# Kernel optimization log

Measured on AMD Instinct MI355X. Metric: run time of the kernel, lower is better.

Reference implementation:

```python
import jax, jax.numpy as jnp
import numpy as np

L, V, D = 8, 512, 256            # num_loci, per-locus vocab, embedding_dim
B, K = 8192, 16                  # batch, candidates per sample
HID = 2 * D                      # pooling MLP hidden width


def setup_inputs() -> dict:
    key = jax.random.key(0)
    k_tok, k_tab, k_w1, k_w2 = jax.random.split(key, 4)
    haplotypes = jax.random.randint(k_tok, (B, K, L), 0, V, dtype=jnp.int64)
    # nn.Embedding default init: N(0, 1); padding_idx row zeroed.
    tables = jax.random.normal(k_tab, (L, V, D), dtype=jnp.float32)
    tables = tables.at[:, 0, :].set(0.0)
    # Xavier-uniform for the two Linear layers (stored as [in, out]).
    lim1 = float(np.sqrt(6.0 / (L * D + HID)))
    W1 = jax.random.uniform(k_w1, (L * D, HID), jnp.float32, -lim1, lim1)
    b1 = jnp.zeros((HID,), jnp.float32)
    lim2 = float(np.sqrt(6.0 / (HID + D)))
    W2 = jax.random.uniform(k_w2, (HID, D), jnp.float32, -lim2, lim2)
    b2 = jnp.zeros((D,), jnp.float32)
    return {"haplotypes": haplotypes, "tables": tables,
            "W1": W1, "b1": b1, "W2": W2, "b2": b2}


def reference(haplotypes, tables, W1, b1, W2, b2):
    b, k, num_loci = haplotypes.shape
    vocab = tables.shape[1]
    tok = jnp.clip(haplotypes.reshape(-1, num_loci), 0, vocab - 1)  # [N, L]
    # Per-locus gather, vectorized over loci: [N, L, D]
    emb = tables[jnp.arange(num_loci), tok]
    # padding_idx row is all-zeros; masking keeps forward identical and
    # matches torch's zero-gradient behavior for the padding row.
    emb = emb * (tok != 0)[..., None].astype(emb.dtype)
    x = emb.reshape(emb.shape[0], num_loci * tables.shape[2])  # concat -> [N, L*D]
    h = jax.nn.gelu(x @ W1 + b1, approximate=False)            # torch GELU = erf
    out = h @ W2 + b2                                          # [N, D]
    return out.reshape(b, k, tables.shape[2])
```

## Files before the change

kernel.cpp:

```cpp
#include <hip/hip_runtime.h>
#include <math.h>

typedef __attribute__((ext_vector_type(8))) short  short8;
typedef __attribute__((ext_vector_type(4))) float  floatx4;
typedef __attribute__((ext_vector_type(2))) float  float2v;
typedef __attribute__((ext_vector_type(4))) unsigned int uintx4;

#define NLOCI 8
#define VOCAB 512
#define DDIM  256
#define HID   512
#define NSAMP (8192 * 16)

__device__ __forceinline__ float bitsf(unsigned int u) {
    union { unsigned int u; float f; } c; c.u = u; return c.f;
}
__device__ __forceinline__ unsigned short f2bf(float f) {
    union { float f; unsigned int u; } c; c.f = f;
    unsigned int u = c.u;
    return (unsigned short)((u + 0x7FFFu + ((u >> 16) & 1u)) >> 16);
}
__device__ __forceinline__ unsigned short f2bf_fast(float f) {
    union { float f; unsigned int u; } c; c.f = f;
    return (unsigned short)((c.u + 0x8000u) >> 16);
}
__device__ __forceinline__ float gelu_fast(float x) {
    float t = x * x;
    float y = x * __builtin_fmaf(0.035677408f, t, 0.79788456f);
    float e = __builtin_amdgcn_exp2f(y * 2.8853901f);
    float r = __builtin_amdgcn_rcpf(e + 1.0f);
    return x - x * r;
}
__device__ __forceinline__ void async_copy16(const void* g, void* l) {
    __builtin_amdgcn_global_load_lds(
        (const __attribute__((address_space(1))) unsigned int*)g,
        (__attribute__((address_space(3))) unsigned int*)l, 16, 0, 0);
}

__global__ __launch_bounds__(256) void k_prep(
    const float* __restrict__ tables,
    const float* __restrict__ W1,
    const float* __restrict__ b1,
    const float* __restrict__ W2,
    unsigned short* __restrict__ Tp,
    unsigned short* __restrict__ W2t)
{
    __shared__ unsigned short a_lds[64 * 256];
    __shared__ unsigned short bt_lds[64 * 256];

    const int t = threadIdx.x;

    if (blockIdx.x >= 512) {
        const int bid = blockIdx.x - 512;
        const int r0 = (bid & 7) * 64;
        const int c0 = (bid >> 3) * 64;
        float* tile = (float*)a_lds;
#pragma unroll
        for (int i = 0; i < 16; ++i) {
            int flat = i * 256 + t;
            int rr = flat >> 6, cc = flat & 63;
            tile[rr * 65 + cc] = W2[(r0 + rr) * DDIM + c0 + cc];
        }
        __syncthreads();
#pragma unroll
        for (int i = 0; i < 8; ++i) {
            int flat = i * 256 + t;
            int cc = flat >> 5, rp = (flat & 31) * 2;
            ushort2 v;
            v.x = f2bf(tile[rp * 65 + cc]);
            v.y = f2bf(tile[(rp + 1) * 65 + cc]);
            *(ushort2*)(W2t + (c0 + cc) * HID + r0 + rp) = v;
        }
        return;
    }

    const int l  = blockIdx.x >> 6;
    const int v0 = ((blockIdx.x >> 3) & 7) * 64;
    const int n0 = (blockIdx.x & 7) * 64;

    {
        const float* asrc = tables + (l * 512 + v0) * 256;
#pragma unroll
        for (int i = 0; i < 16; ++i) {
            int flat = i * 1024 + t * 4;
            int row = flat >> 8, k = flat & 255;
            float4 v = *(const float4*)(asrc + flat);
            ushort4 pk4;
            pk4.x = f2bf(v.x); pk4.y = f2bf(v.y); pk4.z = f2bf(v.z); pk4.w = f2bf(v.w);
            int chunkX = (k >> 3) ^ (row & 31);
            *(ushort4*)(a_lds + row * 256 + chunkX * 8 + (k & 7)) = pk4;
        }
    }
    {
        const int n = t & 63;
        const int kq = (t >> 6) * 64;
        const float* bsrc = W1 + (l * 256) * 512 + n0 + n;
#pragma unroll
        for (int i = 0; i < 8; ++i) {
            int k0 = kq + i * 8;
            short8 pk8;
#pragma unroll
            for (int j = 0; j < 8; ++j)
                pk8[j] = (short)f2bf(bsrc[(k0 + j) * 512]);
            int chunkX = (k0 >> 3) ^ (n & 31);
            *(short8*)(bt_lds + n * 256 + chunkX * 8) = pk8;
        }
    }
    __syncthreads();

    const int wave = t >> 6, lane = t & 63;
    const int p = lane & 15, q = lane >> 4;
    const int arow = wave * 16 + p;

    floatx4 acc[4];
#pragma unroll
    for (int nt = 0; nt < 4; ++nt) acc[nt] = (floatx4){0.f, 0.f, 0.f, 0.f};

#pragma unroll
    for (int kc = 0; kc < 8; ++kc) {
        int cq = kc * 4 + q;
        short8 afrag = *(const short8*)(a_lds + arow * 256 + (cq ^ (arow & 31)) * 8);
#pragma unroll
        for (int nt = 0; nt < 4; ++nt) {
            int brow = nt * 16 + p;
            short8 bfrag = *(const short8*)(bt_lds + brow * 256 + (cq ^ (brow & 31)) * 8);
            acc[nt] = __builtin_amdgcn_mfma_f32_16x16x32_bf16(afrag, bfrag, acc[nt], 0, 0, 0);
        }
    }

#pragma unroll
    for (int nt = 0; nt < 4; ++nt) {
        int col = n0 + nt * 16 + p;
        float badd = (l == 0) ? b1[col] : 0.0f;
#pragma unroll
        for (int r = 0; r < 4; ++r) {
            int row = v0 + wave * 16 + q * 4 + r;
            Tp[(l * 512 + row) * 512 + col] = f2bf(acc[nt][r] + badd);
        }
    }
}

__global__ __launch_bounds__(256, 3) void k_main(
    const int* __restrict__ hap,
    const unsigned short* __restrict__ Tp,
    const unsigned short* __restrict__ W2t,
    const float* __restrict__ b2,
    float* __restrict__ out)
{
    __shared__ unsigned short w2_lds[256 * 64];

    const int t = threadIdx.x;
    const int wave = t >> 6, lane = t & 63;
    const int p = lane & 15, q = lane >> 4;
    const int m_base = blockIdx.x * 64 + wave * 16;

    const char* gbase[8];
    {
        const uintx4* hp = (const uintx4*)(hap + (m_base + p) * 8);
        uintx4 h0 = hp[0], h1 = hp[1];
#pragma unroll
        for (int l = 0; l < 4; ++l) {
            gbase[l]     = (const char*)Tp + (unsigned)l       * 524288u
                         + (h0[l] & 511u) * 1024u + (unsigned)(q * 16);
            gbase[l + 4] = (const char*)Tp + (unsigned)(l + 4) * 524288u
                         + (h1[l] & 511u) * 1024u + (unsigned)(q * 16);
        }
    }

    const int drow = lane >> 3;
    const int j_sw = (lane & 7) ^ (drow & 7);
    const unsigned short* wsrc = W2t + (wave * 64 + drow) * 512 + j_sw * 8;
    const int p7 = p & 7;

    floatx4 acc[16];
#pragma unroll
    for (int nt = 0; nt < 16; ++nt) acc[nt] = (floatx4){0.f, 0.f, 0.f, 0.f};

    uintx4 ga[8], gb[8];
#pragma unroll
    for (int l = 0; l < 8; ++l)
        ga[l] = *(const uintx4*)(gbase[l]);
    __builtin_amdgcn_sched_barrier(0);

#pragma unroll
    for (int s = 0; s < 16; ++s) {
        if ((s & 1) == 0) {
            const int kb = s >> 1;
            asm volatile("s_waitcnt lgkmcnt(0)" ::: "memory");
            __builtin_amdgcn_s_barrier();
            __builtin_amdgcn_sched_barrier(0);
#pragma unroll
            for (int i = 0; i < 8; ++i)
                async_copy16(wsrc + kb * 64 + i * 8 * 512,
                             w2_lds + (wave * 64 + i * 8) * 64);
            __builtin_amdgcn_sched_barrier(0);
        }

        if (s < 15) {
#pragma unroll
            for (int l = 0; l < 8; ++l)
                gb[l] = *(const uintx4*)(gbase[l] + (s + 1) * 64);
            __builtin_amdgcn_sched_barrier(0);
        }

        short8 afrag;
#pragma unroll
        for (int j = 0; j < 4; ++j) {
            float2v u0 = (float2v){bitsf(ga[0][j] << 16), bitsf(ga[0][j] & 0xFFFF0000u)};
            float2v u1 = (float2v){bitsf(ga[1][j] << 16), bitsf(ga[1][j] & 0xFFFF0000u)};
            float2v u2 = (float2v){bitsf(ga[2][j] << 16), bitsf(ga[2][j] & 0xFFFF0000u)};
            float2v u3 = (float2v){bitsf(ga[3][j] << 16), bitsf(ga[3][j] & 0xFFFF0000u)};
            float2v u4 = (float2v){bitsf(ga[4][j] << 16), bitsf(ga[4][j] & 0xFFFF0000u)};
            float2v u5 = (float2v){bitsf(ga[5][j] << 16), bitsf(ga[5][j] & 0xFFFF0000u)};
            float2v u6 = (float2v){bitsf(ga[6][j] << 16), bitsf(ga[6][j] & 0xFFFF0000u)};
            float2v u7 = (float2v){bitsf(ga[7][j] << 16), bitsf(ga[7][j] & 0xFFFF0000u)};
            float2v sj = ((u0 + u1) + (u2 + u3)) + ((u4 + u5) + (u6 + u7));
            afrag[2 * j]     = (short)f2bf_fast(gelu_fast(sj[0]));
            afrag[2 * j + 1] = (short)f2bf_fast(gelu_fast(sj[1]));
        }

        if (s < 15) {
#pragma unroll
            for (int l = 0; l < 8; ++l) ga[l] = gb[l];
        }

        if ((s & 1) == 0) {
            asm volatile("s_waitcnt vmcnt(8)" ::: "memory");
            __builtin_amdgcn_s_barrier();
            __builtin_amdgcn_sched_barrier(0);
        }

        const unsigned short* bbase =
            w2_lds + p * 64 + ((((s & 1) * 4 + q) ^ p7) * 8);
        __builtin_amdgcn_s_setprio(1);
#pragma unroll
        for (int nt = 0; nt < 16; ++nt) {
            short8 bfrag = *(const short8*)(bbase + nt * 1024);
            acc[nt] = __builtin_amdgcn_mfma_f32_16x16x32_bf16(afrag, bfrag, acc[nt], 0, 0, 0);
        }
        __builtin_amdgcn_s_setprio(0);
    }

#pragma unroll
    for (int nt = 0; nt < 16; ++nt) {
        int n = nt * 16 + p;
        float b2v = b2[n];
#pragma unroll
        for (int r = 0; r < 4; ++r) {
            int m = m_base + q * 4 + r;
            __builtin_nontemporal_store(acc[nt][r] + b2v, out + m * 256 + n);
        }
    }
}

extern "C" void kernel_launch(void* const* d_in, const int* in_sizes, int n_in,
                              void* d_out, int out_size, void* d_ws, size_t ws_size,
                              hipStream_t stream) {
    const int*   hap    = (const int*)d_in[0];
    const float* tables = (const float*)d_in[1];
    const float* W1     = (const float*)d_in[2];
    const float* b1     = (const float*)d_in[3];
    const float* W2     = (const float*)d_in[4];
    const float* b2     = (const float*)d_in[5];
    float*       outp   = (float*)d_out;

    unsigned short* Tp  = (unsigned short*)d_ws;
    unsigned short* W2t = (unsigned short*)d_ws + NLOCI * VOCAB * HID;

    k_prep<<<dim3(544), dim3(256), 0, stream>>>(tables, W1, b1, W2, Tp, W2t);
    k_main<<<dim3(NSAMP / 64), dim3(256), 0, stream>>>(hap, Tp, W2t, b2, outp);
}
```

Measured before the change: 286.5 us.

## Restructure gather pipeline to 32-byte contiguous per-lane chunks with split prefetch

```diff
diff --git a/kernel.cpp b/kernel.cpp
--- a/kernel.cpp
+++ b/kernel.cpp
@@ -35,6 +35,25 @@
     __builtin_amdgcn_global_load_lds(
         (const __attribute__((address_space(1))) unsigned int*)g,
         (__attribute__((address_space(3))) unsigned int*)l, 16, 0, 0);
+}
+
+__device__ __forceinline__ short8 sum_gelu(const uintx4* g) {
+    short8 afrag;
+#pragma unroll
+    for (int j = 0; j < 4; ++j) {
+        float2v u0 = (float2v){bitsf(g[0][j] << 16), bitsf(g[0][j] & 0xFFFF0000u)};
+        float2v u1 = (float2v){bitsf(g[1][j] << 16), bitsf(g[1][j] & 0xFFFF0000u)};
+        float2v u2 = (float2v){bitsf(g[2][j] << 16), bitsf(g[2][j] & 0xFFFF0000u)};
+        float2v u3 = (float2v){bitsf(g[3][j] << 16), bitsf(g[3][j] & 0xFFFF0000u)};
+        float2v u4 = (float2v){bitsf(g[4][j] << 16), bitsf(g[4][j] & 0xFFFF0000u)};
+        float2v u5 = (float2v){bitsf(g[5][j] << 16), bitsf(g[5][j] & 0xFFFF0000u)};
+        float2v u6 = (float2v){bitsf(g[6][j] << 16), bitsf(g[6][j] & 0xFFFF0000u)};
+        float2v u7 = (float2v){bitsf(g[7][j] << 16), bitsf(g[7][j] & 0xFFFF0000u)};
+        float2v sj = ((u0 + u1) + (u2 + u3)) + ((u4 + u5) + (u6 + u7));
+        afrag[2 * j]     = (short)f2bf_fast(gelu_fast(sj[0]));
+        afrag[2 * j + 1] = (short)f2bf_fast(gelu_fast(sj[1]));
+    }
+    return afrag;
 }
 
 __global__ __launch_bounds__(256) void k_prep(
@@ -154,18 +173,17 @@
     const int p = lane & 15, q = lane >> 4;
     const int m_base = blockIdx.x * 64 + wave * 16;
 
-    const char* gbase[8];
+    unsigned int goff[8];
     {
         const uintx4* hp = (const uintx4*)(hap + (m_base + p) * 8);
         uintx4 h0 = hp[0], h1 = hp[1];
 #pragma unroll
         for (int l = 0; l < 4; ++l) {
-            gbase[l]     = (const char*)Tp + (unsigned)l       * 524288u
-                         + (h0[l] & 511u) * 1024u + (unsigned)(q * 16);
-            gbase[l + 4] = (const char*)Tp + (unsigned)(l + 4) * 524288u
-                         + (h1[l] & 511u) * 1024u + (unsigned)(q * 16);
-        }
-    }
+            goff[l]     = (unsigned)(l)     * 524288u + (h0[l] & 511u) * 1024u + (unsigned)(q * 32);
+            goff[l + 4] = (unsigned)(l + 4) * 524288u + (h1[l] & 511u) * 1024u + (unsigned)(q * 32);
+        }
+    }
+    const char* Tpc = (const char*)Tp;
 
     const int drow = lane >> 3;
     const int j_sw = (lane & 7) ^ (drow & 7);
@@ -176,69 +194,71 @@
 #pragma unroll
     for (int nt = 0; nt < 16; ++nt) acc[nt] = (floatx4){0.f, 0.f, 0.f, 0.f};
 
-    uintx4 ga[8], gb[8];
+    uintx4 ga0[8], ga1[8];
 #pragma unroll
     for (int l = 0; l < 8; ++l)
-        ga[l] = *(const uintx4*)(gbase[l]);
+        ga0[l] = *(const uintx4*)(Tpc + goff[l]);
+#pragma unroll
+    for (int l = 0; l < 8; ++l)
+        ga1[l] = *(const uintx4*)(Tpc + goff[l] + 16);
     __builtin_amdgcn_sched_barrier(0);
 
 #pragma unroll
-    for (int s = 0; s < 16; ++s) {
-        if ((s & 1) == 0) {
-            const int kb = s >> 1;
-            asm volatile("s_waitcnt lgkmcnt(0)" ::: "memory");
-            __builtin_amdgcn_s_barrier();
+    for (int kb = 0; kb < 8; ++kb) {
+        asm volatile("s_waitcnt lgkmcnt(0)" ::: "memory");
+        __builtin_amdgcn_s_barrier();
+        __builtin_amdgcn_sched_barrier(0);
+#pragma unroll
+        for (int i = 0; i < 8; ++i)
+            async_copy16(wsrc + kb * 64 + i * 8 * 512,
+                         w2_lds + (wave * 64 + i * 8) * 64);
+        __builtin_amdgcn_sched_barrier(0);
+
+        asm volatile("s_waitcnt vmcnt(16)" ::: "memory");
+        short8 afrag0 = sum_gelu(ga0);
+        __builtin_amdgcn_sched_barrier(0);
+
+        if (kb < 7) {
+#pragma unroll
+            for (int l = 0; l < 8; ++l)
+                ga0[l] = *(const uintx4*)(Tpc + goff[l] + (kb + 1) * 128);
             __builtin_amdgcn_sched_barrier(0);
-#pragma unroll
-            for (int i = 0; i < 8; ++i)
-                async_copy16(wsrc + kb * 64 + i * 8 * 512,
-                             w2_lds + (wave * 64 + i * 8) * 64);
+        }
+
+        if (kb < 7) { asm volatile("s_waitcnt vmcnt(8)" ::: "memory"); }
+        else        { asm volatile("s_waitcnt vmcnt(0)" ::: "memory"); }
+        __builtin_amdgcn_s_barrier();
+        __builtin_amdgcn_sched_barrier(0);
+
+        {
+            const unsigned short* b0 = w2_lds + p * 64 + (((q << 1) ^ p7) * 8);
+            __builtin_amdgcn_s_setprio(1);
+#pragma unroll
+            for (int nt = 0; nt < 16; ++nt) {
+                short8 bfrag = *(const short8*)(b0 + nt * 1024);
+                acc[nt] = __builtin_amdgcn_mfma_f32_16x16x32_bf16(afrag0, bfrag, acc[nt], 0, 0, 0);
+            }
+            __builtin_amdgcn_s_setprio(0);
+        }
+
+        short8 afrag1 = sum_gelu(ga1);
+        __builtin_amdgcn_sched_barrier(0);
+        if (kb < 7) {
+#pragma unroll
+            for (int l = 0; l < 8; ++l)
+                ga1[l] = *(const uintx4*)(Tpc + goff[l] + (kb + 1) * 128 + 16);
             __builtin_amdgcn_sched_barrier(0);
         }
-
-        if (s < 15) {
-#pragma unroll
-            for (int l = 0; l < 8; ++l)
-                gb[l] = *(const uintx4*)(gbase[l] + (s + 1) * 64);
-            __builtin_amdgcn_sched_barrier(0);
-        }
-
-        short8 afrag;
-#pragma unroll
-        for (int j = 0; j < 4; ++j) {
-            float2v u0 = (float2v){bitsf(ga[0][j] << 16), bitsf(ga[0][j] & 0xFFFF0000u)};
-            float2v u1 = (float2v){bitsf(ga[1][j] << 16), bitsf(ga[1][j] & 0xFFFF0000u)};
-            float2v u2 = (float2v){bitsf(ga[2][j] << 16), bitsf(ga[2][j] & 0xFFFF0000u)};
-            float2v u3 = (float2v){bitsf(ga[3][j] << 16), bitsf(ga[3][j] & 0xFFFF0000u)};
-            float2v u4 = (float2v){bitsf(ga[4][j] << 16), bitsf(ga[4][j] & 0xFFFF0000u)};
-            float2v u5 = (float2v){bitsf(ga[5][j] << 16), bitsf(ga[5][j] & 0xFFFF0000u)};
-            float2v u6 = (float2v){bitsf(ga[6][j] << 16), bitsf(ga[6][j] & 0xFFFF0000u)};
-            float2v u7 = (float2v){bitsf(ga[7][j] << 16), bitsf(ga[7][j] & 0xFFFF0000u)};
-            float2v sj = ((u0 + u1) + (u2 + u3)) + ((u4 + u5) + (u6 + u7));
-            afrag[2 * j]     = (short)f2bf_fast(gelu_fast(sj[0]));
-            afrag[2 * j + 1] = (short)f2bf_fast(gelu_fast(sj[1]));
-        }
-
-        if (s < 15) {
-#pragma unroll
-            for (int l = 0; l < 8; ++l) ga[l] = gb[l];
-        }
-
-        if ((s & 1) == 0) {
-            asm volatile("s_waitcnt vmcnt(8)" ::: "memory");
-            __builtin_amdgcn_s_barrier();
-            __builtin_amdgcn_sched_barrier(0);
-        }
-
-        const unsigned short* bbase =
-            w2_lds + p * 64 + ((((s & 1) * 4 + q) ^ p7) * 8);
-        __builtin_amdgcn_s_setprio(1);
-#pragma unroll
-        for (int nt = 0; nt < 16; ++nt) {
-            short8 bfrag = *(const short8*)(bbase + nt * 1024);
-            acc[nt] = __builtin_amdgcn_mfma_f32_16x16x32_bf16(afrag, bfrag, acc[nt], 0, 0, 0);
-        }
-        __builtin_amdgcn_s_setprio(0);
+        {
+            const unsigned short* b1p = w2_lds + p * 64 + ((((q << 1) | 1) ^ p7) * 8);
+            __builtin_amdgcn_s_setprio(1);
+#pragma unroll
+            for (int nt = 0; nt < 16; ++nt) {
+                short8 bfrag = *(const short8*)(b1p + nt * 1024);
+                acc[nt] = __builtin_amdgcn_mfma_f32_16x16x32_bf16(afrag1, bfrag, acc[nt], 0, 0, 0);
+            }
+            __builtin_amdgcn_s_setprio(0);
+        }
     }
 
 #pragma unroll
```

Result: no change. 287.9 us (+0.5%).
